# Kernel optimization log

Measured on AMD Instinct MI355X. Metric: run time of the kernel, lower is better.

## Reference

```python
import jax, jax.numpy as jnp
import numpy as np

C, H, W = 512, 192, 192  # feature map dims; 3x3 patches at stride 3 (non-overlapping)


def setup_inputs() -> dict:
    key = jax.random.key(0)
    k1, k2 = jax.random.split(key)
    model_resp = jax.random.normal(k1, (1, C, H, W), dtype=jnp.float32)
    style_resp = jax.random.normal(k2, (1, C, H, W), dtype=jnp.float32)
    return {"model_resp": model_resp, "style_resp": style_resp}


def _unfold3(x):
    # torch.nn.Unfold(kernel=3, stride=3) on (1, C, H, W) -> (C*9, L) after the
    # module's view(patch_count, patch_size) (note: rows are feature channels,
    # columns are spatial locations, matching the original code's dim order).
    _, c, h, w = x.shape
    p = x[0].reshape(c, h // 3, 3, w // 3, 3)          # (c, ph, kh, pw, kw)
    p = p.transpose(0, 2, 4, 1, 3)                      # (c, kh, kw, ph, pw)
    return p.reshape(c * 9, (h // 3) * (w // 3))        # (A, L)


def reference(model_resp, style_resp):
    img = _unfold3(model_resp)                          # (A, L)
    sty = _unfold3(style_resp)                          # (A, L)
    img_norm = 1.0 / jnp.linalg.norm(img, axis=1)       # (A,)
    sty_norm = 1.0 / jnp.linalg.norm(sty, axis=1)       # (A,)
    S = img @ sty.T                                     # (A, A), S[i,j] = img_i . sty_j
    # Faithful to torch: expand(A, A) of a 1-D tensor broadcasts along dim 0,
    # i.e. multiplies COLUMNS by the normalizer vector.
    S1 = S * img_norm[None, :]
    S2 = S1.T * sty_norm[None, :]                       # S2[i,j] = img_norm[i]*sty_norm[j]*(img_j . sty_i)
    nearest = jnp.argmax(S2, axis=0)                    # (A,) int
    max_sim = jnp.max(S2, axis=0)                       # (A,) float (the online-max values)
    return nearest, max_sim
```

## Files before the change

kernel.cpp:

```cpp
#include <hip/hip_runtime.h>
#include <hip/hip_bf16.h>
#include <hip/hip_fp16.h>

#define A_DIM 4608
#define L_DIM 4096
#define CH    512
#define H_DIM 192
#define W_DIM 192

#define BM 128
#define BN 192
#define BK 32
#define NS (L_DIM / BK)

#define CPB 32

typedef _Float16 half8 __attribute__((ext_vector_type(8)));
typedef float   floatx4 __attribute__((ext_vector_type(4)));
typedef float   floatx16 __attribute__((ext_vector_type(16)));

__global__ __launch_bounds__(256) void prep_kernel(
    const float* __restrict__ x0, const float* __restrict__ x1,
    _Float16* __restrict__ Uhi0, _Float16* __restrict__ Ulo0,
    _Float16* __restrict__ Uhi1, _Float16* __restrict__ Ulo1,
    float* __restrict__ ss0, float* __restrict__ ss1) {
  const int which = blockIdx.z;
  const float* __restrict__ x = which ? x1 : x0;
  _Float16* __restrict__ Uhi = which ? Uhi1 : Uhi0;
  _Float16* __restrict__ Ulo = which ? Ulo1 : Ulo0;
  float* __restrict__ ssg = which ? ss1 : ss0;

  const int ph = blockIdx.y;
  const int c0 = blockIdx.x * CPB;
  const int abase = blockIdx.x * (CPB * 9);

  __shared__ _Float16 sHi[CPB * 9 * 8 * 8];
  __shared__ _Float16 sLo[CPB * 9 * 8 * 8];
  __shared__ float ssb[CPB * 9];

  const int t = threadIdx.x;
  for (int a = t; a < CPB * 9; a += 256) ssb[a] = 0.f;
  __syncthreads();

  const int c_l = t >> 3;
  const int s = t & 7;
  const float* __restrict__ rowbase =
      x + ((size_t)(c0 + c_l) * H_DIM + 3 * ph) * W_DIM + s * 24;
  float ssp[9] = {0.f, 0.f, 0.f, 0.f, 0.f, 0.f, 0.f, 0.f, 0.f};

#pragma unroll
  for (int kh = 0; kh < 3; ++kh) {
    const float* __restrict__ rp = rowbase + kh * W_DIM;
    floatx4 v4[6];
#pragma unroll
    for (int i = 0; i < 6; ++i) v4[i] = *(const floatx4*)(rp + i * 4);
    half8 hv[3], lv[3];
#pragma unroll
    for (int i = 0; i < 6; ++i)
#pragma unroll
      for (int j = 0; j < 4; ++j) {
        const int m = i * 4 + j;
        const int kw = m % 3, e = m / 3;
        const float v = v4[i][j];
        ssp[kh * 3 + kw] += v * v;
        const _Float16 h = (_Float16)v;
        hv[kw][e] = h;
        lv[kw][e] = (_Float16)(v - (float)h);
      }
#pragma unroll
    for (int kw = 0; kw < 3; ++kw) {
      const int a_l = c_l * 9 + kh * 3 + kw;
      const int addr = (a_l * 8 + (s ^ (a_l & 7))) * 8;
      *(half8*)&sHi[addr] = hv[kw];
      *(half8*)&sLo[addr] = lv[kw];
    }
  }
#pragma unroll
  for (int q = 0; q < 9; ++q) atomicAdd(&ssb[c_l * 9 + q], ssp[q]);
  __syncthreads();

#pragma unroll
  for (int i = 0; i < 9; ++i) {
    const int idx = i * 256 + t;
    const int c8 = idx / 288;
    const int a_l = idx - c8 * 288;
    const int addr = (a_l * 8 + (c8 ^ (a_l & 7))) * 8;
    const size_t g = ((size_t)(ph * 8 + c8) * A_DIM + abase + a_l) * 8;
    *(half8*)&Uhi[g] = *(const half8*)&sHi[addr];
    *(half8*)&Ulo[g] = *(const half8*)&sLo[addr];
  }
  for (int a = t; a < CPB * 9; a += 256) atomicAdd(&ssg[abase + a], ssb[a]);
}

#define GLDS(g, l)                                                          \
  __builtin_amdgcn_global_load_lds(                                        \
      (const __attribute__((address_space(1))) void*)(g),                   \
      (__attribute__((address_space(3))) void*)(l), 16, 0, 0)

__global__ __launch_bounds__(256, 2) void gemm_max_kernel(
    const _Float16* __restrict__ Shi, const _Float16* __restrict__ Slo,
    const _Float16* __restrict__ Ihi, const _Float16* __restrict__ Ilo,
    const float* __restrict__ img_ss,
    unsigned long long* __restrict__ packed) {
  __shared__ _Float16 sm[2][20480];

  const int t = threadIdx.x;
  const int lane = t & 63, wv = t >> 6;
  const int wvr = wv >> 1, wvc = wv & 1;
  const int id = blockIdx.x;
  const int g = id / 288, r = id - g * 288;
  const int by = r >> 3, bx = g * 8 + (r & 7);
  const int row0 = by * BM;
  const int col0 = bx * BN;
  const int l31 = lane & 31, hs = lane >> 5;

  floatx16 acc[2][3];
#pragma unroll
  for (int rf = 0; rf < 2; ++rf)
#pragma unroll
    for (int cf = 0; cf < 3; ++cf) acc[rf][cf] = (floatx16)0.f;

  const size_t CH8 = (size_t)A_DIM * 8;
  const size_t aOff = (size_t)(t >> 7) * CH8 + (size_t)(row0 + (t & 127)) * 8;
  size_t bOff[3];
#pragma unroll
  for (int i = 0; i < 3; ++i) {
    const int c = i * 256 + t;
    const int kc = c / 192, rw = c - kc * 192;
    bOff[i] = (size_t)kc * CH8 + (size_t)(col0 + rw) * 8;
  }
  const int dl = t * 8;

#define ISSUE(b, koff)                                            \
  do {                                                            \
    GLDS(Shi + (koff) + aOff,           &sm[b][dl]);              \
    GLDS(Shi + (koff) + aOff + 2 * CH8, &sm[b][dl + 2048]);       \
    GLDS(Slo + (koff) + aOff,           &sm[b][4096 + dl]);       \
    GLDS(Slo + (koff) + aOff + 2 * CH8, &sm[b][4096 + dl + 2048]);\
    GLDS(Ihi + (koff) + bOff[0], &sm[b][8192 + dl]);              \
    GLDS(Ihi + (koff) + bOff[1], &sm[b][8192 + dl + 2048]);       \
    GLDS(Ihi + (koff) + bOff[2], &sm[b][8192 + dl + 4096]);       \
    GLDS(Ilo + (koff) + bOff[0], &sm[b][14336 + dl]);             \
    GLDS(Ilo + (koff) + bOff[1], &sm[b][14336 + dl + 2048]);      \
    GLDS(Ilo + (koff) + bOff[2], &sm[b][14336 + dl + 4096]);      \
  } while (0)

  ISSUE(0, 0);

  for (int ks = 0; ks < NS; ++ks) {
    const int cur = ks & 1;
    if (ks + 1 < NS) {
      ISSUE(1 - cur, (size_t)(ks + 1) * 4 * CH8);
      asm volatile("s_waitcnt vmcnt(10)" ::: "memory");
    } else {
      asm volatile("s_waitcnt vmcnt(0)" ::: "memory");
    }
    asm volatile("s_barrier" ::: "memory");

#pragma unroll
    for (int kk = 0; kk < 2; ++kk) {
      const int kc = kk * 2 + hs;
      half8 ah[2], al[2], bh[3], bl[3];
#pragma unroll
      for (int rf = 0; rf < 2; ++rf) {
        const int idx = (kc * 128 + wvr * 64 + rf * 32 + l31) * 8;
        ah[rf] = *(const half8*)&sm[cur][idx];
        al[rf] = *(const half8*)&sm[cur][4096 + idx];
      }
#pragma unroll
      for (int cf = 0; cf < 3; ++cf) {
        const int idx = (kc * 192 + wvc * 96 + cf * 32 + l31) * 8;
        bh[cf] = *(const half8*)&sm[cur][8192 + idx];
        bl[cf] = *(const half8*)&sm[cur][14336 + idx];
      }
#pragma unroll
      for (int rf = 0; rf < 2; ++rf)
#pragma unroll
        for (int cf = 0; cf < 3; ++cf)
          acc[rf][cf] = __builtin_amdgcn_mfma_f32_32x32x16_f16(
              ah[rf], bh[cf], acc[rf][cf], 0, 0, 0);
#pragma unroll
      for (int rf = 0; rf < 2; ++rf)
#pragma unroll
        for (int cf = 0; cf < 3; ++cf)
          acc[rf][cf] = __builtin_amdgcn_mfma_f32_32x32x16_f16(
              ah[rf], bl[cf], acc[rf][cf], 0, 0, 0);
#pragma unroll
      for (int rf = 0; rf < 2; ++rf)
#pragma unroll
        for (int cf = 0; cf < 3; ++cf)
          acc[rf][cf] = __builtin_amdgcn_mfma_f32_32x32x16_f16(
              al[rf], bh[cf], acc[rf][cf], 0, 0, 0);
    }
    asm volatile("s_barrier" ::: "memory");
  }

  float nrv[2][16];
#pragma unroll
  for (int rf = 0; rf < 2; ++rf) {
    const int base_i = row0 + wvr * 64 + rf * 32 + 4 * hs;
#pragma unroll
    for (int g2 = 0; g2 < 4; ++g2) {
      const floatx4 s4 = *(const floatx4*)&img_ss[base_i + 8 * g2];
#pragma unroll
      for (int r2 = 0; r2 < 4; ++r2) nrv[rf][g2 * 4 + r2] = 1.0f / sqrtf(s4[r2]);
    }
  }
#pragma unroll
  for (int cf = 0; cf < 3; ++cf) {
    const int j = col0 + wvc * 96 + cf * 32 + l31;
    float best = -3.4e38f;
    int bi = 0x7FFFFFFF;
#pragma unroll
    for (int rf = 0; rf < 2; ++rf) {
      const int base_i = row0 + wvr * 64 + rf * 32 + 4 * hs;
#pragma unroll
      for (int g2 = 0; g2 < 4; ++g2)
#pragma unroll
        for (int r2 = 0; r2 < 4; ++r2) {
          const int i = base_i + 8 * g2 + r2;
          const float v = acc[rf][cf][g2 * 4 + r2] * nrv[rf][g2 * 4 + r2];
          if (v > best) { best = v; bi = i; }
        }
    }
    const float ov = __shfl_xor(best, 32, 64);
    const int oi = __shfl_xor(bi, 32, 64);
    if (ov > best || (ov == best && oi < bi)) { best = ov; bi = oi; }
    if (hs == 0) {
      const unsigned u = __float_as_uint(best);
      const unsigned key = (u & 0x80000000u) ? ~u : (u | 0x80000000u);
      const unsigned long long pk =
          ((unsigned long long)key << 32) | (unsigned)(~(unsigned)bi);
      atomicMax(&packed[j], pk);
    }
  }
}

__global__ __launch_bounds__(256) void finalize_kernel(
    const unsigned long long* __restrict__ packed,
    const float* __restrict__ sty_ss, float* __restrict__ out) {
  const int j = blockIdx.x * 256 + threadIdx.x;
  if (j >= A_DIM) return;
  const unsigned long long p = packed[j];
  const unsigned key = (unsigned)(p >> 32);
  const unsigned u = (key & 0x80000000u) ? (key ^ 0x80000000u) : ~key;
  const float v = __uint_as_float(u);
  const int idx = (int)(~(unsigned)(p & 0xFFFFFFFFu));
  out[j] = (float)idx;
  out[A_DIM + j] = v * (1.0f / sqrtf(sty_ss[j]));
}

extern "C" void kernel_launch(void* const* d_in, const int* in_sizes, int n_in,
                              void* d_out, int out_size, void* d_ws, size_t ws_size,
                              hipStream_t stream) {
  const float* model = (const float*)d_in[0];
  const float* style = (const float*)d_in[1];
  float* out = (float*)d_out;
  char* ws = (char*)d_ws;

  const size_t usz = (size_t)A_DIM * L_DIM * 2;
  _Float16* img_hi = (_Float16*)(ws);
  _Float16* img_lo = (_Float16*)(ws + usz);
  _Float16* sty_hi = (_Float16*)(ws + 2 * usz);
  _Float16* sty_lo = (_Float16*)(ws + 3 * usz);
  float* img_ss = (float*)(ws + 4 * usz);
  float* sty_ss = img_ss + A_DIM;
  unsigned long long* packed = (unsigned long long*)(img_ss + 2 * A_DIM);

  hipMemsetAsync(img_ss, 0, (size_t)A_DIM * 16, stream);
  prep_kernel<<<dim3(CH / CPB, H_DIM / 3, 2), 256, 0, stream>>>(
      model, style, img_hi, img_lo, sty_hi, sty_lo, img_ss, sty_ss);
  gemm_max_kernel<<<dim3((A_DIM / BM) * (A_DIM / BN)), 256, 0, stream>>>(
      sty_hi, sty_lo, img_hi, img_lo, img_ss, packed);
  finalize_kernel<<<18, 256, 0, stream>>>(packed, sty_ss, out);
}
```

Before: 676.3 us.

## Interleave staged global prefetch with column-fragment MFMA phases and shuffle-reduce sumsq

The GEMM main loop is split into three per-column-fragment phases, each doing its own LDS reads followed by a prioritized block of 12 MFMAs. The next k-step's A, B-hi and B-lo global-to-LDS loads are issued in three separate groups between those phases instead of as one batch, so memory traffic interleaves with compute. Extra barriers, lgkmcnt waits, sched barriers and setprio pin the schedule, which adds synchronization overhead. The prep kernel also replaces the LDS atomic accumulation of sums of squares with an 8-lane shuffle reduction followed by a direct global atomic.

```diff
diff --git a/kernel.cpp b/kernel.cpp
--- a/kernel.cpp
+++ b/kernel.cpp
@@ -36,11 +36,8 @@
 
   __shared__ _Float16 sHi[CPB * 9 * 8 * 8];
   __shared__ _Float16 sLo[CPB * 9 * 8 * 8];
-  __shared__ float ssb[CPB * 9];
 
   const int t = threadIdx.x;
-  for (int a = t; a < CPB * 9; a += 256) ssb[a] = 0.f;
-  __syncthreads();
 
   const int c_l = t >> 3;
   const int s = t & 7;
@@ -76,7 +73,13 @@
     }
   }
 #pragma unroll
-  for (int q = 0; q < 9; ++q) atomicAdd(&ssb[c_l * 9 + q], ssp[q]);
+  for (int q = 0; q < 9; ++q) {
+    float v = ssp[q];
+    v += __shfl_down(v, 4, 8);
+    v += __shfl_down(v, 2, 8);
+    v += __shfl_down(v, 1, 8);
+    if (s == 0) atomicAdd(&ssg[abase + c_l * 9 + q], v);
+  }
   __syncthreads();
 
 #pragma unroll
@@ -89,13 +92,14 @@
     *(half8*)&Uhi[g] = *(const half8*)&sHi[addr];
     *(half8*)&Ulo[g] = *(const half8*)&sLo[addr];
   }
-  for (int a = t; a < CPB * 9; a += 256) atomicAdd(&ssg[abase + a], ssb[a]);
 }
 
 #define GLDS(g, l)                                                          \
   __builtin_amdgcn_global_load_lds(                                        \
       (const __attribute__((address_space(1))) void*)(g),                   \
       (__attribute__((address_space(3))) void*)(l), 16, 0, 0)
+
+#define MFMA_(A, B, C) __builtin_amdgcn_mfma_f32_32x32x16_f16(A, B, C, 0, 0, 0)
 
 __global__ __launch_bounds__(256, 2) void gemm_max_kernel(
     const _Float16* __restrict__ Shi, const _Float16* __restrict__ Slo,
@@ -131,69 +135,125 @@
   }
   const int dl = t * 8;
 
-#define ISSUE(b, koff)                                            \
-  do {                                                            \
-    GLDS(Shi + (koff) + aOff,           &sm[b][dl]);              \
-    GLDS(Shi + (koff) + aOff + 2 * CH8, &sm[b][dl + 2048]);       \
-    GLDS(Slo + (koff) + aOff,           &sm[b][4096 + dl]);       \
-    GLDS(Slo + (koff) + aOff + 2 * CH8, &sm[b][4096 + dl + 2048]);\
-    GLDS(Ihi + (koff) + bOff[0], &sm[b][8192 + dl]);              \
-    GLDS(Ihi + (koff) + bOff[1], &sm[b][8192 + dl + 2048]);       \
-    GLDS(Ihi + (koff) + bOff[2], &sm[b][8192 + dl + 4096]);       \
-    GLDS(Ilo + (koff) + bOff[0], &sm[b][14336 + dl]);             \
-    GLDS(Ilo + (koff) + bOff[1], &sm[b][14336 + dl + 2048]);      \
-    GLDS(Ilo + (koff) + bOff[2], &sm[b][14336 + dl + 4096]);      \
+#define G_A(b, koff)                                               \
+  do {                                                             \
+    GLDS(Shi + (koff) + aOff,           &sm[b][dl]);               \
+    GLDS(Shi + (koff) + aOff + 2 * CH8, &sm[b][dl + 2048]);        \
+    GLDS(Slo + (koff) + aOff,           &sm[b][4096 + dl]);        \
+    GLDS(Slo + (koff) + aOff + 2 * CH8, &sm[b][4096 + dl + 2048]); \
   } while (0)
-
-  ISSUE(0, 0);
-
-  for (int ks = 0; ks < NS; ++ks) {
-    const int cur = ks & 1;
-    if (ks + 1 < NS) {
-      ISSUE(1 - cur, (size_t)(ks + 1) * 4 * CH8);
-      asm volatile("s_waitcnt vmcnt(10)" ::: "memory");
+#define G_BH(b, koff)                                              \
+  do {                                                             \
+    GLDS(Ihi + (koff) + bOff[0], &sm[b][8192 + dl]);               \
+    GLDS(Ihi + (koff) + bOff[1], &sm[b][8192 + dl + 2048]);        \
+    GLDS(Ihi + (koff) + bOff[2], &sm[b][8192 + dl + 4096]);        \
+  } while (0)
+#define G_BL(b, koff)                                              \
+  do {                                                             \
+    GLDS(Ilo + (koff) + bOff[0], &sm[b][14336 + dl]);              \
+    GLDS(Ilo + (koff) + bOff[1], &sm[b][14336 + dl + 2048]);       \
+    GLDS(Ilo + (koff) + bOff[2], &sm[b][14336 + dl + 4096]);       \
+  } while (0)
+
+#define BARRIER asm volatile("s_barrier" ::: "memory")
+#define LGKM0 asm volatile("s_waitcnt lgkmcnt(0)" ::: "memory")
+#define SCHED0 __builtin_amdgcn_sched_barrier(0)
+
+#define MM12(CF, BH0, BL0, BH1, BL1)                      \
+  do {                                                    \
+    acc[0][CF] = MFMA_(ah0[0], BH0, acc[0][CF]);          \
+    acc[1][CF] = MFMA_(ah0[1], BH0, acc[1][CF]);          \
+    acc[0][CF] = MFMA_(ah0[0], BL0, acc[0][CF]);          \
+    acc[1][CF] = MFMA_(ah0[1], BL0, acc[1][CF]);          \
+    acc[0][CF] = MFMA_(al0[0], BH0, acc[0][CF]);          \
+    acc[1][CF] = MFMA_(al0[1], BH0, acc[1][CF]);          \
+    acc[0][CF] = MFMA_(ah1[0], BH1, acc[0][CF]);          \
+    acc[1][CF] = MFMA_(ah1[1], BH1, acc[1][CF]);          \
+    acc[0][CF] = MFMA_(ah1[0], BL1, acc[0][CF]);          \
+    acc[1][CF] = MFMA_(ah1[1], BL1, acc[1][CF]);          \
+    acc[0][CF] = MFMA_(al1[0], BH1, acc[0][CF]);          \
+    acc[1][CF] = MFMA_(al1[1], BH1, acc[1][CF]);          \
+  } while (0)
+
+  const int aA = ((hs)*128 + wvr * 64 + l31) * 8;
+  const int aB = ((2 + hs) * 128 + wvr * 64 + l31) * 8;
+  const int bA = ((hs)*192 + wvc * 96 + l31) * 8;
+  const int bB = ((2 + hs) * 192 + wvc * 96 + l31) * 8;
+
+  G_A(0, 0);
+  G_BH(0, 0);
+  G_BL(0, 0);
+
+  auto kstep = [&](int cur, bool pf, size_t koff) {
+    const int nxt = cur ^ 1;
+    if (pf) {
+      G_A(nxt, koff);
+      asm volatile("s_waitcnt vmcnt(4)" ::: "memory");
     } else {
       asm volatile("s_waitcnt vmcnt(0)" ::: "memory");
     }
-    asm volatile("s_barrier" ::: "memory");
-
-#pragma unroll
-    for (int kk = 0; kk < 2; ++kk) {
-      const int kc = kk * 2 + hs;
-      half8 ah[2], al[2], bh[3], bl[3];
-#pragma unroll
-      for (int rf = 0; rf < 2; ++rf) {
-        const int idx = (kc * 128 + wvr * 64 + rf * 32 + l31) * 8;
-        ah[rf] = *(const half8*)&sm[cur][idx];
-        al[rf] = *(const half8*)&sm[cur][4096 + idx];
-      }
-#pragma unroll
-      for (int cf = 0; cf < 3; ++cf) {
-        const int idx = (kc * 192 + wvc * 96 + cf * 32 + l31) * 8;
-        bh[cf] = *(const half8*)&sm[cur][8192 + idx];
-        bl[cf] = *(const half8*)&sm[cur][14336 + idx];
-      }
-#pragma unroll
-      for (int rf = 0; rf < 2; ++rf)
-#pragma unroll
-        for (int cf = 0; cf < 3; ++cf)
-          acc[rf][cf] = __builtin_amdgcn_mfma_f32_32x32x16_f16(
-              ah[rf], bh[cf], acc[rf][cf], 0, 0, 0);
-#pragma unroll
-      for (int rf = 0; rf < 2; ++rf)
-#pragma unroll
-        for (int cf = 0; cf < 3; ++cf)
-          acc[rf][cf] = __builtin_amdgcn_mfma_f32_32x32x16_f16(
-              ah[rf], bl[cf], acc[rf][cf], 0, 0, 0);
-#pragma unroll
-      for (int rf = 0; rf < 2; ++rf)
-#pragma unroll
-        for (int cf = 0; cf < 3; ++cf)
-          acc[rf][cf] = __builtin_amdgcn_mfma_f32_32x32x16_f16(
-              al[rf], bh[cf], acc[rf][cf], 0, 0, 0);
-    }
-    asm volatile("s_barrier" ::: "memory");
-  }
+    BARRIER;
+
+    const _Float16* __restrict__ S = &sm[cur][0];
+    half8 ah0[2], al0[2], ah1[2], al1[2];
+
+    ah0[0] = *(const half8*)&S[aA];
+    ah0[1] = *(const half8*)&S[aA + 256];
+    al0[0] = *(const half8*)&S[4096 + aA];
+    al0[1] = *(const half8*)&S[4096 + aA + 256];
+    ah1[0] = *(const half8*)&S[aB];
+    ah1[1] = *(const half8*)&S[aB + 256];
+    al1[0] = *(const half8*)&S[4096 + aB];
+    al1[1] = *(const half8*)&S[4096 + aB + 256];
+    {
+      half8 bh0 = *(const half8*)&S[8192 + bA];
+      half8 bl0 = *(const half8*)&S[14336 + bA];
+      half8 bh1 = *(const half8*)&S[8192 + bB];
+      half8 bl1 = *(const half8*)&S[14336 + bB];
+      if (pf) G_BH(nxt, koff);
+      BARRIER;
+      LGKM0;
+      SCHED0;
+      __builtin_amdgcn_s_setprio(1);
+      MM12(0, bh0, bl0, bh1, bl1);
+      __builtin_amdgcn_s_setprio(0);
+      SCHED0;
+      BARRIER;
+    }
+    {
+      half8 bh0 = *(const half8*)&S[8192 + bA + 256];
+      half8 bl0 = *(const half8*)&S[14336 + bA + 256];
+      half8 bh1 = *(const half8*)&S[8192 + bB + 256];
+      half8 bl1 = *(const half8*)&S[14336 + bB + 256];
+      if (pf) G_BL(nxt, koff);
+      BARRIER;
+      LGKM0;
+      SCHED0;
+      __builtin_amdgcn_s_setprio(1);
+      MM12(1, bh0, bl0, bh1, bl1);
+      __builtin_amdgcn_s_setprio(0);
+      SCHED0;
+      BARRIER;
+    }
+    {
+      half8 bh0 = *(const half8*)&S[8192 + bA + 512];
+      half8 bl0 = *(const half8*)&S[14336 + bA + 512];
+      half8 bh1 = *(const half8*)&S[8192 + bB + 512];
+      half8 bl1 = *(const half8*)&S[14336 + bB + 512];
+      BARRIER;
+      LGKM0;
+      SCHED0;
+      __builtin_amdgcn_s_setprio(1);
+      MM12(2, bh0, bl0, bh1, bl1);
+      __builtin_amdgcn_s_setprio(0);
+      SCHED0;
+      BARRIER;
+    }
+  };
+
+  for (int ks = 0; ks < NS - 1; ++ks)
+    kstep(ks & 1, true, (size_t)(ks + 1) * 4 * CH8);
+  kstep((NS - 1) & 1, false, 0);
 
   float nrv[2][16];
 #pragma unroll
```

After: 652.3 us. 3.6% less time.

## Use triple-buffered BK=16 LDS pipeline with single barrier per step; shuffle-reduce norms

Applied to the files above, without the earlier changes.

The GEMM main loop moves from a double-buffered BK=32 scheme to a triple-buffered BK=16 ring. Loads are issued two stages ahead, and each k-step needs only one barrier instead of two. This is meant to overlap global-to-LDS transfers with MFMA work better and cut barrier stalls, at the cost of twice as many loop iterations and smaller per-step compute. The prep kernel also drops its shared-memory atomic accumulation of squared norms in favour of warp shuffles and direct global atomics.

```diff
diff --git a/kernel.cpp b/kernel.cpp
--- a/kernel.cpp
+++ b/kernel.cpp
@@ -10,7 +10,7 @@
 
 #define BM 128
 #define BN 192
-#define BK 32
+#define BK 16
 #define NS (L_DIM / BK)
 
 #define CPB 32
@@ -36,11 +36,8 @@
 
   __shared__ _Float16 sHi[CPB * 9 * 8 * 8];
   __shared__ _Float16 sLo[CPB * 9 * 8 * 8];
-  __shared__ float ssb[CPB * 9];
 
   const int t = threadIdx.x;
-  for (int a = t; a < CPB * 9; a += 256) ssb[a] = 0.f;
-  __syncthreads();
 
   const int c_l = t >> 3;
   const int s = t & 7;
@@ -76,7 +73,13 @@
     }
   }
 #pragma unroll
-  for (int q = 0; q < 9; ++q) atomicAdd(&ssb[c_l * 9 + q], ssp[q]);
+  for (int q = 0; q < 9; ++q) {
+    float v = ssp[q];
+    v += __shfl_down(v, 4, 8);
+    v += __shfl_down(v, 2, 8);
+    v += __shfl_down(v, 1, 8);
+    if (s == 0) atomicAdd(&ssg[abase + c_l * 9 + q], v);
+  }
   __syncthreads();
 
 #pragma unroll
@@ -89,20 +92,21 @@
     *(half8*)&Uhi[g] = *(const half8*)&sHi[addr];
     *(half8*)&Ulo[g] = *(const half8*)&sLo[addr];
   }
-  for (int a = t; a < CPB * 9; a += 256) atomicAdd(&ssg[abase + a], ssb[a]);
 }
 
 #define GLDS(g, l)                                                          \
   __builtin_amdgcn_global_load_lds(                                        \
       (const __attribute__((address_space(1))) void*)(g),                   \
       (__attribute__((address_space(3))) void*)(l), 16, 0, 0)
+
+#define MFMA_(A, B, C) __builtin_amdgcn_mfma_f32_32x32x16_f16(A, B, C, 0, 0, 0)
 
 __global__ __launch_bounds__(256, 2) void gemm_max_kernel(
     const _Float16* __restrict__ Shi, const _Float16* __restrict__ Slo,
     const _Float16* __restrict__ Ihi, const _Float16* __restrict__ Ilo,
     const float* __restrict__ img_ss,
     unsigned long long* __restrict__ packed) {
-  __shared__ _Float16 sm[2][20480];
+  __shared__ _Float16 sm[3 * 10240];
 
   const int t = threadIdx.x;
   const int lane = t & 63, wv = t >> 6;
@@ -121,78 +125,79 @@
     for (int cf = 0; cf < 3; ++cf) acc[rf][cf] = (floatx16)0.f;
 
   const size_t CH8 = (size_t)A_DIM * 8;
+
   const size_t aOff = (size_t)(t >> 7) * CH8 + (size_t)(row0 + (t & 127)) * 8;
-  size_t bOff[3];
-#pragma unroll
-  for (int i = 0; i < 3; ++i) {
-    const int c = i * 256 + t;
-    const int kc = c / 192, rw = c - kc * 192;
-    bOff[i] = (size_t)kc * CH8 + (size_t)(col0 + rw) * 8;
-  }
-  const int dl = t * 8;
-
-#define ISSUE(b, koff)                                            \
-  do {                                                            \
-    GLDS(Shi + (koff) + aOff,           &sm[b][dl]);              \
-    GLDS(Shi + (koff) + aOff + 2 * CH8, &sm[b][dl + 2048]);       \
-    GLDS(Slo + (koff) + aOff,           &sm[b][4096 + dl]);       \
-    GLDS(Slo + (koff) + aOff + 2 * CH8, &sm[b][4096 + dl + 2048]);\
-    GLDS(Ihi + (koff) + bOff[0], &sm[b][8192 + dl]);              \
-    GLDS(Ihi + (koff) + bOff[1], &sm[b][8192 + dl + 2048]);       \
-    GLDS(Ihi + (koff) + bOff[2], &sm[b][8192 + dl + 4096]);       \
-    GLDS(Ilo + (koff) + bOff[0], &sm[b][14336 + dl]);             \
-    GLDS(Ilo + (koff) + bOff[1], &sm[b][14336 + dl + 2048]);      \
-    GLDS(Ilo + (koff) + bOff[2], &sm[b][14336 + dl + 4096]);      \
+  const int aDst = t * 8;
+  const size_t bG0 =
+      (size_t)(t / 192) * CH8 + (size_t)(col0 + (t % 192)) * 8;
+  const int bD0 = 4096 + t * 8;
+  const int c1 = 256 + t;
+  const int mat1 = (c1 >= 384) ? 1 : 0;
+  const int rem1 = c1 - mat1 * 384;
+  const _Float16* __restrict__ bP1 = mat1 ? Ilo : Ihi;
+  const size_t bG1 =
+      (size_t)(rem1 / 192) * CH8 + (size_t)(col0 + (rem1 % 192)) * 8;
+  const int bD1 = 4096 + mat1 * 3072 + rem1 * 8;
+  const int rem2 = 128 + t;
+  const size_t bG2 =
+      (size_t)(rem2 / 192) * CH8 + (size_t)(col0 + (rem2 % 192)) * 8;
+  const int bD2 = 7168 + rem2 * 8;
+
+#define ISSUE(BB, koff)                                  \
+  do {                                                   \
+    GLDS(Shi + (koff) + aOff, &sm[(BB) + aDst]);         \
+    GLDS(Slo + (koff) + aOff, &sm[(BB) + 2048 + aDst]);  \
+    GLDS(Ihi + (koff) + bG0, &sm[(BB) + bD0]);           \
+    GLDS(bP1 + (koff) + bG1, &sm[(BB) + bD1]);           \
+    GLDS(Ilo + (koff) + bG2, &sm[(BB) + bD2]);           \
   } while (0)
 
+  const int aI = (hs * 128 + wvr * 64 + l31) * 8;
+  const int bI = (hs * 192 + wvc * 96 + l31) * 8;
+
   ISSUE(0, 0);
-
+  ISSUE(10240, 2 * CH8);
+
+  int bufC = 0, bufP = 20480;
   for (int ks = 0; ks < NS; ++ks) {
-    const int cur = ks & 1;
-    if (ks + 1 < NS) {
-      ISSUE(1 - cur, (size_t)(ks + 1) * 4 * CH8);
-      asm volatile("s_waitcnt vmcnt(10)" ::: "memory");
+    if (ks < NS - 1) {
+      asm volatile("s_waitcnt vmcnt(5)" ::: "memory");
     } else {
       asm volatile("s_waitcnt vmcnt(0)" ::: "memory");
     }
     asm volatile("s_barrier" ::: "memory");
 
-#pragma unroll
-    for (int kk = 0; kk < 2; ++kk) {
-      const int kc = kk * 2 + hs;
-      half8 ah[2], al[2], bh[3], bl[3];
-#pragma unroll
-      for (int rf = 0; rf < 2; ++rf) {
-        const int idx = (kc * 128 + wvr * 64 + rf * 32 + l31) * 8;
-        ah[rf] = *(const half8*)&sm[cur][idx];
-        al[rf] = *(const half8*)&sm[cur][4096 + idx];
-      }
-#pragma unroll
-      for (int cf = 0; cf < 3; ++cf) {
-        const int idx = (kc * 192 + wvc * 96 + cf * 32 + l31) * 8;
-        bh[cf] = *(const half8*)&sm[cur][8192 + idx];
-        bl[cf] = *(const half8*)&sm[cur][14336 + idx];
-      }
-#pragma unroll
-      for (int rf = 0; rf < 2; ++rf)
-#pragma unroll
-        for (int cf = 0; cf < 3; ++cf)
-          acc[rf][cf] = __builtin_amdgcn_mfma_f32_32x32x16_f16(
-              ah[rf], bh[cf], acc[rf][cf], 0, 0, 0);
-#pragma unroll
-      for (int rf = 0; rf < 2; ++rf)
-#pragma unroll
-        for (int cf = 0; cf < 3; ++cf)
-          acc[rf][cf] = __builtin_amdgcn_mfma_f32_32x32x16_f16(
-              ah[rf], bl[cf], acc[rf][cf], 0, 0, 0);
-#pragma unroll
-      for (int rf = 0; rf < 2; ++rf)
-#pragma unroll
-        for (int cf = 0; cf < 3; ++cf)
-          acc[rf][cf] = __builtin_amdgcn_mfma_f32_32x32x16_f16(
-              al[rf], bh[cf], acc[rf][cf], 0, 0, 0);
-    }
-    asm volatile("s_barrier" ::: "memory");
+    if (ks + 2 < NS) ISSUE(bufP, (size_t)(ks + 2) * 2 * CH8);
+
+    half8 ah[2], al[2], bh[3], bl[3];
+#pragma unroll
+    for (int rf = 0; rf < 2; ++rf) {
+      ah[rf] = *(const half8*)&sm[bufC + aI + rf * 256];
+      al[rf] = *(const half8*)&sm[bufC + 2048 + aI + rf * 256];
+    }
+#pragma unroll
+    for (int cf = 0; cf < 3; ++cf) {
+      bh[cf] = *(const half8*)&sm[bufC + 4096 + bI + cf * 256];
+      bl[cf] = *(const half8*)&sm[bufC + 7168 + bI + cf * 256];
+    }
+#pragma unroll
+    for (int rf = 0; rf < 2; ++rf)
+#pragma unroll
+      for (int cf = 0; cf < 3; ++cf)
+        acc[rf][cf] = MFMA_(ah[rf], bh[cf], acc[rf][cf]);
+#pragma unroll
+    for (int rf = 0; rf < 2; ++rf)
+#pragma unroll
+      for (int cf = 0; cf < 3; ++cf)
+        acc[rf][cf] = MFMA_(ah[rf], bl[cf], acc[rf][cf]);
+#pragma unroll
+    for (int rf = 0; rf < 2; ++rf)
+#pragma unroll
+      for (int cf = 0; cf < 3; ++cf)
+        acc[rf][cf] = MFMA_(al[rf], bh[cf], acc[rf][cf]);
+
+    bufC = (bufC == 20480) ? 0 : bufC + 10240;
+    bufP = (bufP == 20480) ? 0 : bufP + 10240;
   }
 
   float nrv[2][16];
```

Measured after the change: 676.6 us. No clear change (+0.0%).
